# Optimization experiments

Measured on AMD Instinct MI355X. Metric: run time of the kernel, lower is better.

The kernel has to match this reference:

```python
import jax, jax.numpy as jnp
import numpy as np

SCOPE = 2
N = 20
D = 64
CAP = 32
IN_CH = 64
OUT_CH = 64
FIN_CH = 64
WIDTH = 2 * SCOPE + 1


def setup_inputs() -> dict:
    key = jax.random.key(0)
    ks = jax.random.split(key, 7)
    dm = 3 * CAP + D  # memory feature dim: 3 relpos blocks + spatial embedding

    def w(k, fan_in, shape):
        return jax.random.normal(k, shape, jnp.float32) / np.sqrt(fan_in)

    return dict(
        spatial_embeddings=jax.random.normal(ks[0], (N, N, N, D), jnp.float32),
        relpos_w=jax.random.normal(ks[1], (WIDTH, CAP), jnp.float32) / np.sqrt(WIDTH * CAP),
        Wq=w(ks[2], D, (D, IN_CH)), bq=jnp.zeros((IN_CH,), jnp.float32),
        Wk=w(ks[3], dm, (dm, IN_CH)), bk=jnp.zeros((IN_CH,), jnp.float32),
        Wv=w(ks[4], dm, (dm, OUT_CH)), bv=jnp.zeros((OUT_CH,), jnp.float32),
        Wo=w(ks[5], OUT_CH, (OUT_CH, FIN_CH)), bo=jnp.zeros((FIN_CH,), jnp.float32),
    )


def reference(spatial_embeddings, relpos_w, Wq, bq, Wk, bk, Wv, bv, Wo, bo):
    n = spatial_embeddings.shape[0]
    w = WIDTH
    m = n + 2 * SCOPE  # padded grid size
    cap = relpos_w.shape[-1]

    # within_edges=False: zero-pad all three spatial axes by SCOPE
    se = jnp.pad(spatial_embeddings, ((SCOPE, SCOPE),) * 3 + ((0, 0),))
    central = SCOPE + jnp.arange(n)               # padded centre indices [n]
    off = jnp.arange(-SCOPE, SCOPE + 1)           # [w]
    idx = central[:, None] + off[None, :]         # [n, w] padded neighbour indices

    # relative-position cube: relpos_cube[x,y,z] = concat(r[x], r[y], r[z])
    r0 = jnp.broadcast_to(relpos_w[:, None, None, :], (w, w, w, cap))
    r1 = jnp.broadcast_to(relpos_w[None, :, None, :], (w, w, w, cap))
    r2 = jnp.broadcast_to(relpos_w[None, None, :, :], (w, w, w, cap))
    relpos_flat = jnp.concatenate([r0, r1, r2], axis=-1).reshape(w * w * w, 3 * cap)

    # neighbour gather replicating jnp.meshgrid(...)'s default 'xy' indexing:
    # cube[b, a, c] = se[ni[a], nj[b], nk[c]]
    ii = idx[:, None, None, None, :, None]        # (qi, a)
    jj = idx[None, :, None, :, None, None]        # (qj, b)
    kk = idx[None, None, :, None, None, :]        # (qk, c)
    nb = se[ii, jj, kk]                           # [n,n,n,w,w,w,D]
    nb = nb.reshape(n, n, n, w * w * w, -1)       # [n,n,n,w^3,D]

    # keys/values over memory = concat(relpos, neighbours); split the weight
    Wk_rel, Wk_nb = Wk[:3 * cap], Wk[3 * cap:]
    Wv_rel, Wv_nb = Wv[:3 * cap], Wv[3 * cap:]
    k_rel = relpos_flat @ Wk_rel + bk             # [w^3, IN_CH] (query-independent)
    v_rel = relpos_flat @ Wv_rel + bv             # [w^3, OUT_CH]
    keys = k_rel + jnp.einsum('xyzpd,dc->xyzpc', nb, Wk_nb)
    values = v_rel + jnp.einsum('xyzpd,dc->xyzpc', nb, Wv_nb)

    # centre embedding at padded index `central` == original unpadded embedding
    q = spatial_embeddings @ Wq + bq              # [n,n,n,IN_CH]
    logits = jnp.einsum('xyzc,xyzpc->xyzp', q, keys)

    # edge mask, built in (a,b,c) cube order (faithful to original's flatten order)
    valid = ((idx > SCOPE) & (idx < m - SCOPE)).astype(logits.dtype)  # [n, w]
    mask = (valid[:, None, None, :, None, None]
            * valid[None, :, None, None, :, None]
            * valid[None, None, :, None, None, :]).reshape(n, n, n, w * w * w)
    logits = logits - (1.0 - mask) * 1e9

    scores = jax.nn.softmax(logits, axis=-1)
    reweighted = jnp.einsum('xyzp,xyzpc->xyzc', scores, values)
    return reweighted @ Wo + bo                   # [n,n,n,FIN_CH]
```

## Files before the change

### kernel.cpp

```cpp
#include <hip/hip_runtime.h>

#define NN 20
#define NP 125
#define NV (NN*NN*NN)

__global__ __launch_bounds__(64) void prep(
        const float* __restrict__ rpw,
        const float* __restrict__ Wk, const float* __restrict__ bk,
        const float* __restrict__ Wv, const float* __restrict__ bv,
        const float* __restrict__ Wo,
        float* __restrict__ k_rel, float* __restrict__ vrelW,
        float* __restrict__ Wvo) {
    const int c = threadIdx.x;
    if (blockIdx.x < NP) {
        const int p = blockIdx.x;
        const int d3 = p / 25, d4 = (p / 5) % 5, d5 = p % 5;
        __shared__ float vtmp[64];
        float ak = bk[c], av = bv[c];
#pragma unroll
        for (int t = 0; t < 96; ++t) {
            const int blk = t >> 5, off = t & 31;
            const int row = (blk == 0) ? d3 : (blk == 1) ? d4 : d5;
            const float r = rpw[row * 32 + off];
            ak = fmaf(r, Wk[t * 64 + c], ak);
            av = fmaf(r, Wv[t * 64 + c], av);
        }
        k_rel[p * 64 + c] = ak;
        vtmp[c] = av;
        __syncthreads();
        float o = 0.f;
#pragma unroll 8
        for (int e = 0; e < 64; ++e)
            o = fmaf(vtmp[e], Wo[e * 64 + c], o);
        vrelW[p * 64 + c] = o;
    } else {
        const int d = blockIdx.x - NP;
        float acc = 0.f;
#pragma unroll 8
        for (int e = 0; e < 64; ++e)
            acc = fmaf(Wv[(96 + d) * 64 + e], Wo[e * 64 + c], acc);
        Wvo[d * 64 + c] = acc;
    }
}

__global__ __launch_bounds__(256) void qkv2(
        const float* __restrict__ SE,
        const float* __restrict__ Wq, const float* __restrict__ bq,
        const float* __restrict__ Wk, const float* __restrict__ Wvo,
        float* __restrict__ Q, float* __restrict__ Km, float* __restrict__ VW) {
    __shared__ float se_s[32][65];
    const int t = threadIdx.x;
    const int vbase = blockIdx.x * 32;
    {
        const float4* __restrict__ src = (const float4*)(SE + vbase * 64);
        const float4 a = src[t];
        const float4 b = src[t + 256];
        const int r0 = t >> 4,        c0 = (t & 15) * 4;
        const int r1 = (t + 256) >> 4;
        se_s[r0][c0 + 0] = a.x; se_s[r0][c0 + 1] = a.y;
        se_s[r0][c0 + 2] = a.z; se_s[r0][c0 + 3] = a.w;
        se_s[r1][c0 + 0] = b.x; se_s[r1][c0 + 1] = b.y;
        se_s[r1][c0 + 2] = b.z; se_s[r1][c0 + 3] = b.w;
    }
    __syncthreads();
    const int lane = t & 63, w = t >> 6;
    float aq[8], ak[8], av[8];
#pragma unroll
    for (int j = 0; j < 8; ++j) { aq[j] = bq[lane]; ak[j] = 0.f; av[j] = 0.f; }
#pragma unroll 8
    for (int d = 0; d < 64; ++d) {
        const float wq = Wq[d * 64 + lane];
        const float wk = Wk[(96 + d) * 64 + lane];
        const float wv = Wvo[d * 64 + lane];
#pragma unroll
        for (int j = 0; j < 8; ++j) {
            const float s = se_s[w * 8 + j][d];
            aq[j] = fmaf(s, wq, aq[j]);
            ak[j] = fmaf(s, wk, ak[j]);
            av[j] = fmaf(s, wv, av[j]);
        }
    }
#pragma unroll
    for (int j = 0; j < 8; ++j) {
        const int v = vbase + w * 8 + j;
        Q[v * 64 + lane]  = aq[j];
        Km[v * 64 + lane] = ak[j];
        VW[v * 64 + lane] = av[j];
    }
}

__global__ __launch_bounds__(512, 4) void attn4(
        const float* __restrict__ Q, const float* __restrict__ Km,
        const float* __restrict__ VW,
        const float* __restrict__ k_rel, const float* __restrict__ vrelW,
        const float* __restrict__ bo,
        float* __restrict__ out) {
    __shared__ float u[216 * 65];
    __shared__ float sc_s[8][128];

    const int tid  = threadIdx.x;
    const int lane = tid & 63;
    const int w    = tid >> 6;

    const int chunk = blockIdx.x & 7;
    const int idx   = blockIdx.x >> 3;
    const int cx = chunk >> 2, cy = (chunk >> 1) & 1, cz = chunk & 1;
    const int TX = cx * 5 + idx / 25;
    const int TY = cy * 5 + (idx / 5) % 5;
    const int TZ = cz * 5 + idx % 5;

    const int wx = w >> 2, wy = (w >> 1) & 1, wz = w & 1;
    const int x = TX * 2 + wx, y = TY * 2 + wy, z = TZ * 2 + wz;
    const int v = (x * NN + y) * NN + z;

    for (int i = tid; i < 216 * 16; i += 512) {
        const int row = i >> 4, ch = i & 15;
        const int ux = row / 36, uy = (row / 6) % 6, uz = row % 6;
        const int gX = TX * 2 - 2 + ux;
        const int gY = TY * 2 - 2 + uy;
        const int gZ = TZ * 2 - 2 + uz;
        float4 val = make_float4(0.f, 0.f, 0.f, 0.f);
        if ((unsigned)gX <= 19u && (unsigned)gY <= 19u && (unsigned)gZ <= 19u)
            val = ((const float4*)Km)[((gX * NN + gY) * NN + gZ) * 16 + ch];
        const int b = row * 65 + ch * 4;
        u[b] = val.x; u[b + 1] = val.y; u[b + 2] = val.z; u[b + 3] = val.w;
    }

    const float q = Q[v * 64 + lane];
    const int p0 = lane;
    const int p1 = lane + 64;
    const int p1c = (p1 < NP) ? p1 : (NP - 1);

    int e3 = p0 / 25, e4 = (p0 / 5) % 5, e5 = p0 % 5;
    const int row0 = 36 * (wx + e4) + 6 * (wy + e3) + (wz + e5);
    const bool mv0 = ((unsigned)(x + e3 - 3) <= 18u) &&
                     ((unsigned)(y + e4 - 3) <= 18u) &&
                     ((unsigned)(z + e5 - 3) <= 18u);
    e3 = p1c / 25; e4 = (p1c / 5) % 5; e5 = p1c % 5;
    const int row1 = 36 * (wx + e4) + 6 * (wy + e3) + (wz + e5);
    const bool mv1 = (p1 < NP) &&
                     ((unsigned)(x + e3 - 3) <= 18u) &&
                     ((unsigned)(y + e4 - 3) <= 18u) &&
                     ((unsigned)(z + e5 - 3) <= 18u);

    const float4* __restrict__ kr0 = (const float4*)(k_rel + p0 * 64);
    const float4* __restrict__ kr1 = (const float4*)(k_rel + p1c * 64);

    __syncthreads();

    float a0 = 0.f, a1 = 0.f;
#pragma unroll
    for (int i = 0; i < 16; ++i) {
        const float qa = __shfl(q, 4 * i + 0);
        const float qb = __shfl(q, 4 * i + 1);
        const float qc = __shfl(q, 4 * i + 2);
        const float qd = __shfl(q, 4 * i + 3);
        const float4 r0 = kr0[i], r1 = kr1[i];
        const int b0 = row0 * 65 + 4 * i;
        const int b1 = row1 * 65 + 4 * i;
        a0 = fmaf(u[b0] + r0.x, qa, a0);
        a0 = fmaf(u[b0 + 1] + r0.y, qb, a0);
        a0 = fmaf(u[b0 + 2] + r0.z, qc, a0);
        a0 = fmaf(u[b0 + 3] + r0.w, qd, a0);
        a1 = fmaf(u[b1] + r1.x, qa, a1);
        a1 = fmaf(u[b1 + 1] + r1.y, qb, a1);
        a1 = fmaf(u[b1 + 2] + r1.z, qc, a1);
        a1 = fmaf(u[b1 + 3] + r1.w, qd, a1);
    }
    const float l0 = mv0 ? a0 : -1e9f;
    const float l1 = mv1 ? a1 : -1e9f;

    float m = fmaxf(l0, l1);
#pragma unroll
    for (int d = 1; d < 64; d <<= 1) m = fmaxf(m, __shfl_xor(m, d));
    const float e0 = __expf(l0 - m);
    const float e1 = __expf(l1 - m);
    float ssum = e0 + e1;
#pragma unroll
    for (int d = 1; d < 64; d <<= 1) ssum += __shfl_xor(ssum, d);
    const float inv = 1.f / ssum;
    sc_s[w][p0] = e0 * inv;
    sc_s[w][p1] = e1 * inv;
    __syncthreads();

    for (int i = tid; i < 216 * 16; i += 512) {
        const int row = i >> 4, ch = i & 15;
        const int ux = row / 36, uy = (row / 6) % 6, uz = row % 6;
        const int gX = TX * 2 - 2 + ux;
        const int gY = TY * 2 - 2 + uy;
        const int gZ = TZ * 2 - 2 + uz;
        float4 val = make_float4(0.f, 0.f, 0.f, 0.f);
        if ((unsigned)gX <= 19u && (unsigned)gY <= 19u && (unsigned)gZ <= 19u)
            val = ((const float4*)VW)[((gX * NN + gY) * NN + gZ) * 16 + ch];
        const int b = row * 65 + ch * 4;
        u[b] = val.x; u[b + 1] = val.y; u[b + 2] = val.z; u[b + 3] = val.w;
    }
    __syncthreads();

    float A0 = 0.f, A1 = 0.f, A2 = 0.f, A3 = 0.f, A4 = 0.f;
    const float* __restrict__ vr = vrelW + lane;
#pragma unroll 5
    for (int g = 0; g < 25; ++g) {
        const int ge3 = g / 5, ge4 = g % 5;
        const int rb = 36 * (wx + ge4) + 6 * (wy + ge3) + wz;
        const int pb = g * 5;
        A0 = fmaf(sc_s[w][pb + 0], u[(rb + 0) * 65 + lane] + vr[(pb + 0) * 64], A0);
        A1 = fmaf(sc_s[w][pb + 1], u[(rb + 1) * 65 + lane] + vr[(pb + 1) * 64], A1);
        A2 = fmaf(sc_s[w][pb + 2], u[(rb + 2) * 65 + lane] + vr[(pb + 2) * 64], A2);
        A3 = fmaf(sc_s[w][pb + 3], u[(rb + 3) * 65 + lane] + vr[(pb + 3) * 64], A3);
        A4 = fmaf(sc_s[w][pb + 4], u[(rb + 4) * 65 + lane] + vr[(pb + 4) * 64], A4);
    }
    const float rw = ((A0 + A1) + (A2 + A3)) + A4;
    out[v * 64 + lane] = rw + bo[lane];
}

extern "C" void kernel_launch(void* const* d_in, const int* in_sizes, int n_in,
                              void* d_out, int out_size, void* d_ws, size_t ws_size,
                              hipStream_t stream) {
    const float* SE  = (const float*)d_in[0];
    const float* rpw = (const float*)d_in[1];
    const float* Wq  = (const float*)d_in[2];
    const float* bq  = (const float*)d_in[3];
    const float* Wk  = (const float*)d_in[4];
    const float* bk  = (const float*)d_in[5];
    const float* Wv  = (const float*)d_in[6];
    const float* bv  = (const float*)d_in[7];
    const float* Wo  = (const float*)d_in[8];
    const float* bo  = (const float*)d_in[9];
    float* out = (float*)d_out;

    float* ws    = (float*)d_ws;
    float* Q     = ws;
    float* Km    = ws + 512000;
    float* VW    = ws + 1024000;
    float* k_rel = ws + 1536000;
    float* vrelW = ws + 1544000;
    float* Wvo   = ws + 1552000;

    prep<<<NP + 64, 64, 0, stream>>>(rpw, Wk, bk, Wv, bv, Wo, k_rel, vrelW, Wvo);
    qkv2<<<NV / 32, 256, 0, stream>>>(SE, Wq, bq, Wk, Wvo, Q, Km, VW);
    attn4<<<1000, 512, 0, stream>>>(Q, Km, VW, k_rel, vrelW, bo, out);
}
```

Baseline: 134.9 us.

## Merge prep and projection kernels; read neighbour values directly from global memory

The separate prep and qkv kernels become one launch. Each projection block recomputes the Wv·Wo product into shared memory, while the extra blocks compute k_rel and vrelW four positions per block. In the attention kernel, the shared-memory staging of the 216-row VW halo is dropped and each lane loads its neighbour values straight from global memory with bounds predicates. This removes a launch and a barrier plus the staging loop. In exchange, every block redundantly recomputes Wvo, and the value gather now relies on global/L2 traffic instead of shared memory.

```diff
diff --git a/kernel.cpp b/kernel.cpp
--- a/kernel.cpp
+++ b/kernel.cpp
@@ -4,92 +4,93 @@
 #define NP 125
 #define NV (NN*NN*NN)
 
-__global__ __launch_bounds__(64) void prep(
-        const float* __restrict__ rpw,
+__global__ __launch_bounds__(256) void pre(
+        const float* __restrict__ SE, const float* __restrict__ rpw,
+        const float* __restrict__ Wq, const float* __restrict__ bq,
         const float* __restrict__ Wk, const float* __restrict__ bk,
         const float* __restrict__ Wv, const float* __restrict__ bv,
         const float* __restrict__ Wo,
-        float* __restrict__ k_rel, float* __restrict__ vrelW,
-        float* __restrict__ Wvo) {
-    const int c = threadIdx.x;
-    if (blockIdx.x < NP) {
-        const int p = blockIdx.x;
-        const int d3 = p / 25, d4 = (p / 5) % 5, d5 = p % 5;
-        __shared__ float vtmp[64];
-        float ak = bk[c], av = bv[c];
-#pragma unroll
-        for (int t = 0; t < 96; ++t) {
-            const int blk = t >> 5, off = t & 31;
+        float* __restrict__ Q, float* __restrict__ Km, float* __restrict__ VW,
+        float* __restrict__ k_rel, float* __restrict__ vrelW) {
+    const int t = threadIdx.x;
+    const int lane = t & 63, w = t >> 6;
+
+    if (blockIdx.x < 500) {
+        __shared__ float se_s[16][65];
+        __shared__ float wvo_s[64 * 65];
+        const int vbase = blockIdx.x * 16;
+        {
+            const float4 a = ((const float4*)(SE + vbase * 64))[t];
+            const int r0 = t >> 4, c0 = (t & 15) * 4;
+            se_s[r0][c0 + 0] = a.x; se_s[r0][c0 + 1] = a.y;
+            se_s[r0][c0 + 2] = a.z; se_s[r0][c0 + 3] = a.w;
+        }
+        float acc[16];
+#pragma unroll
+        for (int k = 0; k < 16; ++k) acc[k] = 0.f;
+#pragma unroll 4
+        for (int e = 0; e < 64; ++e) {
+            const float wo = Wo[e * 64 + lane];
+#pragma unroll
+            for (int k = 0; k < 16; ++k)
+                acc[k] = fmaf(Wv[(96 + w * 16 + k) * 64 + e], wo, acc[k]);
+        }
+#pragma unroll
+        for (int k = 0; k < 16; ++k)
+            wvo_s[(w * 16 + k) * 65 + lane] = acc[k];
+        __syncthreads();
+
+        float aq[4], ak[4], av[4];
+#pragma unroll
+        for (int j = 0; j < 4; ++j) { aq[j] = bq[lane]; ak[j] = 0.f; av[j] = 0.f; }
+#pragma unroll 8
+        for (int d = 0; d < 64; ++d) {
+            const float wq = Wq[d * 64 + lane];
+            const float wk = Wk[(96 + d) * 64 + lane];
+            const float wv = wvo_s[d * 65 + lane];
+#pragma unroll
+            for (int j = 0; j < 4; ++j) {
+                const float s = se_s[w * 4 + j][d];
+                aq[j] = fmaf(s, wq, aq[j]);
+                ak[j] = fmaf(s, wk, ak[j]);
+                av[j] = fmaf(s, wv, av[j]);
+            }
+        }
+#pragma unroll
+        for (int j = 0; j < 4; ++j) {
+            const int v = vbase + w * 4 + j;
+            Q[v * 64 + lane]  = aq[j];
+            Km[v * 64 + lane] = ak[j];
+            VW[v * 64 + lane] = av[j];
+        }
+    } else {
+        __shared__ float vt[4][65];
+        const int p = (blockIdx.x - 500) * 4 + w;
+        const int pc = (p < NP) ? p : (NP - 1);
+        const int d3 = pc / 25, d4 = (pc / 5) % 5, d5 = pc % 5;
+        float ak = bk[lane], av = bv[lane];
+#pragma unroll
+        for (int tt = 0; tt < 96; ++tt) {
+            const int blk = tt >> 5, off = tt & 31;
             const int row = (blk == 0) ? d3 : (blk == 1) ? d4 : d5;
             const float r = rpw[row * 32 + off];
-            ak = fmaf(r, Wk[t * 64 + c], ak);
-            av = fmaf(r, Wv[t * 64 + c], av);
-        }
-        k_rel[p * 64 + c] = ak;
-        vtmp[c] = av;
+            ak = fmaf(r, Wk[tt * 64 + lane], ak);
+            av = fmaf(r, Wv[tt * 64 + lane], av);
+        }
+        vt[w][lane] = av;
         __syncthreads();
         float o = 0.f;
-#pragma unroll 8
+#pragma unroll 4
         for (int e = 0; e < 64; ++e)
-            o = fmaf(vtmp[e], Wo[e * 64 + c], o);
-        vrelW[p * 64 + c] = o;
-    } else {
-        const int d = blockIdx.x - NP;
-        float acc = 0.f;
-#pragma unroll 8
-        for (int e = 0; e < 64; ++e)
-            acc = fmaf(Wv[(96 + d) * 64 + e], Wo[e * 64 + c], acc);
-        Wvo[d * 64 + c] = acc;
+            o = fmaf(vt[w][e], Wo[e * 64 + lane], o);
+        if (p < NP) {
+            k_rel[p * 64 + lane] = ak;
+            vrelW[p * 64 + lane] = o;
+        }
     }
 }
 
-__global__ __launch_bounds__(256) void qkv2(
-        const float* __restrict__ SE,
-        const float* __restrict__ Wq, const float* __restrict__ bq,
-        const float* __restrict__ Wk, const float* __restrict__ Wvo,
-        float* __restrict__ Q, float* __restrict__ Km, float* __restrict__ VW) {
-    __shared__ float se_s[32][65];
-    const int t = threadIdx.x;
-    const int vbase = blockIdx.x * 32;
-    {
-        const float4* __restrict__ src = (const float4*)(SE + vbase * 64);
-        const float4 a = src[t];
-        const float4 b = src[t + 256];
-        const int r0 = t >> 4,        c0 = (t & 15) * 4;
-        const int r1 = (t + 256) >> 4;
-        se_s[r0][c0 + 0] = a.x; se_s[r0][c0 + 1] = a.y;
-        se_s[r0][c0 + 2] = a.z; se_s[r0][c0 + 3] = a.w;
-        se_s[r1][c0 + 0] = b.x; se_s[r1][c0 + 1] = b.y;
-        se_s[r1][c0 + 2] = b.z; se_s[r1][c0 + 3] = b.w;
-    }
-    __syncthreads();
-    const int lane = t & 63, w = t >> 6;
-    float aq[8], ak[8], av[8];
-#pragma unroll
-    for (int j = 0; j < 8; ++j) { aq[j] = bq[lane]; ak[j] = 0.f; av[j] = 0.f; }
-#pragma unroll 8
-    for (int d = 0; d < 64; ++d) {
-        const float wq = Wq[d * 64 + lane];
-        const float wk = Wk[(96 + d) * 64 + lane];
-        const float wv = Wvo[d * 64 + lane];
-#pragma unroll
-        for (int j = 0; j < 8; ++j) {
-            const float s = se_s[w * 8 + j][d];
-            aq[j] = fmaf(s, wq, aq[j]);
-            ak[j] = fmaf(s, wk, ak[j]);
-            av[j] = fmaf(s, wv, av[j]);
-        }
-    }
-#pragma unroll
-    for (int j = 0; j < 8; ++j) {
-        const int v = vbase + w * 8 + j;
-        Q[v * 64 + lane]  = aq[j];
-        Km[v * 64 + lane] = ak[j];
-        VW[v * 64 + lane] = av[j];
-    }
-}
-
-__global__ __launch_bounds__(512, 4) void attn4(
+__global__ __launch_bounds__(512, 4) void attn5(
         const float* __restrict__ Q, const float* __restrict__ Km,
         const float* __restrict__ VW,
         const float* __restrict__ k_rel, const float* __restrict__ vrelW,
@@ -183,32 +184,42 @@
     sc_s[w][p1] = e1 * inv;
     __syncthreads();
 
-    for (int i = tid; i < 216 * 16; i += 512) {
-        const int row = i >> 4, ch = i & 15;
-        const int ux = row / 36, uy = (row / 6) % 6, uz = row % 6;
-        const int gX = TX * 2 - 2 + ux;
-        const int gY = TY * 2 - 2 + uy;
-        const int gZ = TZ * 2 - 2 + uz;
-        float4 val = make_float4(0.f, 0.f, 0.f, 0.f);
-        if ((unsigned)gX <= 19u && (unsigned)gY <= 19u && (unsigned)gZ <= 19u)
-            val = ((const float4*)VW)[((gX * NN + gY) * NN + gZ) * 16 + ch];
-        const int b = row * 65 + ch * 4;
-        u[b] = val.x; u[b + 1] = val.y; u[b + 2] = val.z; u[b + 3] = val.w;
-    }
-    __syncthreads();
-
+    bool xin[5], yin[5], zin[5];
+#pragma unroll
+    for (int o = 0; o < 5; ++o) {
+        xin[o] = ((unsigned)(x + o - 2) <= 19u);
+        yin[o] = ((unsigned)(y + o - 2) <= 19u);
+        zin[o] = ((unsigned)(z + o - 2) <= 19u);
+    }
     float A0 = 0.f, A1 = 0.f, A2 = 0.f, A3 = 0.f, A4 = 0.f;
     const float* __restrict__ vr = vrelW + lane;
+    const float* __restrict__ vwl = VW + lane;
 #pragma unroll 5
     for (int g = 0; g < 25; ++g) {
         const int ge3 = g / 5, ge4 = g % 5;
-        const int rb = 36 * (wx + ge4) + 6 * (wy + ge3) + wz;
+        const int nbb = v + (ge4 - 2) * 400 + (ge3 - 2) * 20 - 2;
+        const bool xy = xin[ge4] && yin[ge3];
         const int pb = g * 5;
-        A0 = fmaf(sc_s[w][pb + 0], u[(rb + 0) * 65 + lane] + vr[(pb + 0) * 64], A0);
-        A1 = fmaf(sc_s[w][pb + 1], u[(rb + 1) * 65 + lane] + vr[(pb + 1) * 64], A1);
-        A2 = fmaf(sc_s[w][pb + 2], u[(rb + 2) * 65 + lane] + vr[(pb + 2) * 64], A2);
-        A3 = fmaf(sc_s[w][pb + 3], u[(rb + 3) * 65 + lane] + vr[(pb + 3) * 64], A3);
-        A4 = fmaf(sc_s[w][pb + 4], u[(rb + 4) * 65 + lane] + vr[(pb + 4) * 64], A4);
+        {
+            const float vm = (xy && zin[0]) ? vwl[(nbb + 0) * 64] : 0.f;
+            A0 = fmaf(sc_s[w][pb + 0], vr[(pb + 0) * 64] + vm, A0);
+        }
+        {
+            const float vm = (xy && zin[1]) ? vwl[(nbb + 1) * 64] : 0.f;
+            A1 = fmaf(sc_s[w][pb + 1], vr[(pb + 1) * 64] + vm, A1);
+        }
+        {
+            const float vm = (xy && zin[2]) ? vwl[(nbb + 2) * 64] : 0.f;
+            A2 = fmaf(sc_s[w][pb + 2], vr[(pb + 2) * 64] + vm, A2);
+        }
+        {
+            const float vm = (xy && zin[3]) ? vwl[(nbb + 3) * 64] : 0.f;
+            A3 = fmaf(sc_s[w][pb + 3], vr[(pb + 3) * 64] + vm, A3);
+        }
+        {
+            const float vm = (xy && zin[4]) ? vwl[(nbb + 4) * 64] : 0.f;
+            A4 = fmaf(sc_s[w][pb + 4], vr[(pb + 4) * 64] + vm, A4);
+        }
     }
     const float rw = ((A0 + A1) + (A2 + A3)) + A4;
     out[v * 64 + lane] = rw + bo[lane];
@@ -235,9 +246,8 @@
     float* VW    = ws + 1024000;
     float* k_rel = ws + 1536000;
     float* vrelW = ws + 1544000;
-    float* Wvo   = ws + 1552000;
-
-    prep<<<NP + 64, 64, 0, stream>>>(rpw, Wk, bk, Wv, bv, Wo, k_rel, vrelW, Wvo);
-    qkv2<<<NV / 32, 256, 0, stream>>>(SE, Wq, bq, Wk, Wvo, Q, Km, VW);
-    attn4<<<1000, 512, 0, stream>>>(Q, Km, VW, k_rel, vrelW, bo, out);
+
+    pre<<<532, 256, 0, stream>>>(SE, rpw, Wq, bq, Wk, bk, Wv, bv, Wo,
+                                 Q, Km, VW, k_rel, vrelW);
+    attn5<<<1000, 512, 0, stream>>>(Q, Km, VW, k_rel, vrelW, bo, out);
 }
```

Measured after the change: 151.8 us. +12.5%, slower.

## Split each voxel's 125 neighbours across two wavefronts with 1024-thread blocks

Applied to the files above, without the earlier changes.

The attention kernel now uses 1024 threads per block, so two wavefronts share each voxel. Each wavefront computes 64 of the 125 neighbour logits, and the softmax max and sum are combined across the pair through shared memory. The weighted value sum is split the same way, with the two halves added through shared memory before the store. This doubles thread-level parallelism and shortens each wave's serial work, at the cost of extra barriers, half-idle lanes in the second wave (61 of 64 used), and higher register pressure under launch_bounds(1024,2).

```diff
diff --git a/kernel.cpp b/kernel.cpp
--- a/kernel.cpp
+++ b/kernel.cpp
@@ -89,18 +89,21 @@
     }
 }
 
-__global__ __launch_bounds__(512, 4) void attn4(
+__global__ __launch_bounds__(1024, 2) void attn6(
         const float* __restrict__ Q, const float* __restrict__ Km,
         const float* __restrict__ VW,
         const float* __restrict__ k_rel, const float* __restrict__ vrelW,
         const float* __restrict__ bo,
         float* __restrict__ out) {
     __shared__ float u[216 * 65];
-    __shared__ float sc_s[8][128];
+    __shared__ float mred[16], sred[16];
+    __shared__ float prw[8][64];
 
     const int tid  = threadIdx.x;
     const int lane = tid & 63;
     const int w    = tid >> 6;
+    const int vox  = w & 7;
+    const int hi   = w >> 3;
 
     const int chunk = blockIdx.x & 7;
     const int idx   = blockIdx.x >> 3;
@@ -109,11 +112,11 @@
     const int TY = cy * 5 + (idx / 5) % 5;
     const int TZ = cz * 5 + idx % 5;
 
-    const int wx = w >> 2, wy = (w >> 1) & 1, wz = w & 1;
+    const int wx = vox >> 2, wy = (vox >> 1) & 1, wz = vox & 1;
     const int x = TX * 2 + wx, y = TY * 2 + wy, z = TZ * 2 + wz;
     const int v = (x * NN + y) * NN + z;
 
-    for (int i = tid; i < 216 * 16; i += 512) {
+    for (int i = tid; i < 216 * 16; i += 1024) {
         const int row = i >> 4, ch = i & 15;
         const int ux = row / 36, uy = (row / 6) % 6, uz = row % 6;
         const int gX = TX * 2 - 2 + ux;
@@ -127,63 +130,42 @@
     }
 
     const float q = Q[v * 64 + lane];
-    const int p0 = lane;
-    const int p1 = lane + 64;
-    const int p1c = (p1 < NP) ? p1 : (NP - 1);
-
-    int e3 = p0 / 25, e4 = (p0 / 5) % 5, e5 = p0 % 5;
-    const int row0 = 36 * (wx + e4) + 6 * (wy + e3) + (wz + e5);
-    const bool mv0 = ((unsigned)(x + e3 - 3) <= 18u) &&
-                     ((unsigned)(y + e4 - 3) <= 18u) &&
-                     ((unsigned)(z + e5 - 3) <= 18u);
-    e3 = p1c / 25; e4 = (p1c / 5) % 5; e5 = p1c % 5;
-    const int row1 = 36 * (wx + e4) + 6 * (wy + e3) + (wz + e5);
-    const bool mv1 = (p1 < NP) &&
-                     ((unsigned)(x + e3 - 3) <= 18u) &&
-                     ((unsigned)(y + e4 - 3) <= 18u) &&
-                     ((unsigned)(z + e5 - 3) <= 18u);
-
-    const float4* __restrict__ kr0 = (const float4*)(k_rel + p0 * 64);
-    const float4* __restrict__ kr1 = (const float4*)(k_rel + p1c * 64);
-
-    __syncthreads();
-
-    float a0 = 0.f, a1 = 0.f;
+
+    const int p  = lane + hi * 64;
+    const int pc = (p < NP) ? p : (NP - 1);
+    const int e3 = pc / 25, e4 = (pc / 5) % 5, e5 = pc % 5;
+    const int rowp = 36 * (wx + e4) + 6 * (wy + e3) + (wz + e5);
+    const bool mv = (p < NP) &&
+                    ((unsigned)(x + e3 - 3) <= 18u) &&
+                    ((unsigned)(y + e4 - 3) <= 18u) &&
+                    ((unsigned)(z + e5 - 3) <= 18u);
+    const float4* __restrict__ kr = (const float4*)(k_rel + pc * 64);
+
+    __syncthreads();
+
+    float a = 0.f;
 #pragma unroll
     for (int i = 0; i < 16; ++i) {
         const float qa = __shfl(q, 4 * i + 0);
         const float qb = __shfl(q, 4 * i + 1);
         const float qc = __shfl(q, 4 * i + 2);
         const float qd = __shfl(q, 4 * i + 3);
-        const float4 r0 = kr0[i], r1 = kr1[i];
-        const int b0 = row0 * 65 + 4 * i;
-        const int b1 = row1 * 65 + 4 * i;
-        a0 = fmaf(u[b0] + r0.x, qa, a0);
-        a0 = fmaf(u[b0 + 1] + r0.y, qb, a0);
-        a0 = fmaf(u[b0 + 2] + r0.z, qc, a0);
-        a0 = fmaf(u[b0 + 3] + r0.w, qd, a0);
-        a1 = fmaf(u[b1] + r1.x, qa, a1);
-        a1 = fmaf(u[b1 + 1] + r1.y, qb, a1);
-        a1 = fmaf(u[b1 + 2] + r1.z, qc, a1);
-        a1 = fmaf(u[b1 + 3] + r1.w, qd, a1);
-    }
-    const float l0 = mv0 ? a0 : -1e9f;
-    const float l1 = mv1 ? a1 : -1e9f;
-
-    float m = fmaxf(l0, l1);
+        const float4 r = kr[i];
+        const int b = rowp * 65 + 4 * i;
+        a = fmaf(u[b]     + r.x, qa, a);
+        a = fmaf(u[b + 1] + r.y, qb, a);
+        a = fmaf(u[b + 2] + r.z, qc, a);
+        a = fmaf(u[b + 3] + r.w, qd, a);
+    }
+    const float l = mv ? a : -1e9f;
+
+    float m = l;
 #pragma unroll
     for (int d = 1; d < 64; d <<= 1) m = fmaxf(m, __shfl_xor(m, d));
-    const float e0 = __expf(l0 - m);
-    const float e1 = __expf(l1 - m);
-    float ssum = e0 + e1;
-#pragma unroll
-    for (int d = 1; d < 64; d <<= 1) ssum += __shfl_xor(ssum, d);
-    const float inv = 1.f / ssum;
-    sc_s[w][p0] = e0 * inv;
-    sc_s[w][p1] = e1 * inv;
-    __syncthreads();
-
-    for (int i = tid; i < 216 * 16; i += 512) {
+    if (lane == 0) mred[w] = m;
+    __syncthreads();
+
+    for (int i = tid; i < 216 * 16; i += 1024) {
         const int row = i >> 4, ch = i & 15;
         const int ux = row / 36, uy = (row / 6) % 6, uz = row % 6;
         const int gX = TX * 2 - 2 + ux;
@@ -195,23 +177,46 @@
         const int b = row * 65 + ch * 4;
         u[b] = val.x; u[b + 1] = val.y; u[b + 2] = val.z; u[b + 3] = val.w;
     }
-    __syncthreads();
+
+    const float mm = fmaxf(mred[vox], mred[vox + 8]);
+    const float e  = __expf(l - mm);
+    float s = e;
+#pragma unroll
+    for (int d = 1; d < 64; d <<= 1) s += __shfl_xor(s, d);
+    if (lane == 0) sred[w] = s;
+    __syncthreads();
+
+    const float inv = 1.f / (sred[vox] + sred[vox + 8]);
+    const float sc_mine = e * inv;
 
     float A0 = 0.f, A1 = 0.f, A2 = 0.f, A3 = 0.f, A4 = 0.f;
     const float* __restrict__ vr = vrelW + lane;
-#pragma unroll 5
-    for (int g = 0; g < 25; ++g) {
-        const int ge3 = g / 5, ge4 = g % 5;
-        const int rb = 36 * (wx + ge4) + 6 * (wy + ge3) + wz;
-        const int pb = g * 5;
-        A0 = fmaf(sc_s[w][pb + 0], u[(rb + 0) * 65 + lane] + vr[(pb + 0) * 64], A0);
-        A1 = fmaf(sc_s[w][pb + 1], u[(rb + 1) * 65 + lane] + vr[(pb + 1) * 64], A1);
-        A2 = fmaf(sc_s[w][pb + 2], u[(rb + 2) * 65 + lane] + vr[(pb + 2) * 64], A2);
-        A3 = fmaf(sc_s[w][pb + 3], u[(rb + 3) * 65 + lane] + vr[(pb + 3) * 64], A3);
-        A4 = fmaf(sc_s[w][pb + 4], u[(rb + 4) * 65 + lane] + vr[(pb + 4) * 64], A4);
-    }
-    const float rw = ((A0 + A1) + (A2 + A3)) + A4;
-    out[v * 64 + lane] = rw + bo[lane];
+    if (hi == 0) {
+#pragma unroll
+        for (int pp = 0; pp < 64; ++pp) {
+            const int f3 = pp / 25, f4 = (pp / 5) % 5, f5 = pp % 5;
+            const int row = 36 * (wx + f4) + 6 * (wy + f3) + (wz + f5);
+            const float sc = __shfl(sc_mine, pp);
+            float& A = (pp % 5 == 0) ? A0 : (pp % 5 == 1) ? A1 :
+                       (pp % 5 == 2) ? A2 : (pp % 5 == 3) ? A3 : A4;
+            A = fmaf(sc, u[row * 65 + lane] + vr[pp * 64], A);
+        }
+    } else {
+#pragma unroll
+        for (int pp = 64; pp < NP; ++pp) {
+            const int f3 = pp / 25, f4 = (pp / 5) % 5, f5 = pp % 5;
+            const int row = 36 * (wx + f4) + 6 * (wy + f3) + (wz + f5);
+            const float sc = __shfl(sc_mine, pp - 64);
+            float& A = (pp % 5 == 0) ? A0 : (pp % 5 == 1) ? A1 :
+                       (pp % 5 == 2) ? A2 : (pp % 5 == 3) ? A3 : A4;
+            A = fmaf(sc, u[row * 65 + lane] + vr[pp * 64], A);
+        }
+    }
+    const float part = ((A0 + A1) + (A2 + A3)) + A4;
+    if (hi == 1) prw[vox][lane] = part;
+    __syncthreads();
+    if (hi == 0)
+        out[v * 64 + lane] = part + prw[vox][lane] + bo[lane];
 }
 
 extern "C" void kernel_launch(void* const* d_in, const int* in_sizes, int n_in,
@@ -239,5 +244,5 @@
 
     prep<<<NP + 64, 64, 0, stream>>>(rpw, Wk, bk, Wv, bv, Wo, k_rel, vrelW, Wvo);
     qkv2<<<NV / 32, 256, 0, stream>>>(SE, Wq, bq, Wk, Wvo, Q, Km, VW);
-    attn4<<<1000, 512, 0, stream>>>(Q, Km, VW, k_rel, vrelW, bo, out);
-}
+    attn6<<<1000, 1024, 0, stream>>>(Q, Km, VW, k_rel, vrelW, bo, out);
+}
```

Result: slower. 148.7 us (+10.3%).

## Precompute q·k_rel in projection kernel and score over 216 shared neighbour rows

Applied to the files above, without the earlier changes.

The q·k_rel term is now computed once per voxel in the projection kernel and written to a workspace buffer, so the attention kernel no longer adds relpos keys per element. Each wave computes dot products over all 216 rows of the shared key tile with float4 LDS reads (stride 68), and then maps them back to the 125 window positions through shuffles. Softmax scores stay in registers and are broadcast with readlane instead of passing through shared memory. In exchange, the projection kernel does extra work and more global writes (qkr is 128 floats per voxel), and the attention kernel does about 1.7x more dot-product FLOPs on out-of-window rows. Occupancy drops from launch bound 4 to 2.

```diff
diff --git a/kernel.cpp b/kernel.cpp
--- a/kernel.cpp
+++ b/kernel.cpp
@@ -3,6 +3,10 @@
 #define NN 20
 #define NP 125
 #define NV (NN*NN*NN)
+
+__device__ __forceinline__ float rlf(float v, int l) {
+    return __uint_as_float(__builtin_amdgcn_readlane(__float_as_uint(v), l));
+}
 
 __global__ __launch_bounds__(64) void prep(
         const float* __restrict__ rpw,
@@ -43,12 +47,15 @@
     }
 }
 
-__global__ __launch_bounds__(256) void qkv2(
+__global__ __launch_bounds__(256) void qkv3(
         const float* __restrict__ SE,
         const float* __restrict__ Wq, const float* __restrict__ bq,
         const float* __restrict__ Wk, const float* __restrict__ Wvo,
-        float* __restrict__ Q, float* __restrict__ Km, float* __restrict__ VW) {
+        const float* __restrict__ k_rel,
+        float* __restrict__ Q, float* __restrict__ Km, float* __restrict__ VW,
+        float* __restrict__ qkr) {
     __shared__ float se_s[32][65];
+    __shared__ float krs[125 * 65];
     const int t = threadIdx.x;
     const int vbase = blockIdx.x * 32;
     {
@@ -62,6 +69,12 @@
         se_s[r1][c0 + 0] = b.x; se_s[r1][c0 + 1] = b.y;
         se_s[r1][c0 + 2] = b.z; se_s[r1][c0 + 3] = b.w;
     }
+    for (int i = t; i < 125 * 16; i += 256) {
+        const int row = i >> 4, ch = i & 15;
+        const float4 val = ((const float4*)k_rel)[row * 16 + ch];
+        const int b = row * 65 + ch * 4;
+        krs[b] = val.x; krs[b + 1] = val.y; krs[b + 2] = val.z; krs[b + 3] = val.w;
+    }
     __syncthreads();
     const int lane = t & 63, w = t >> 6;
     float aq[8], ak[8], av[8];
@@ -87,16 +100,35 @@
         Km[v * 64 + lane] = ak[j];
         VW[v * 64 + lane] = av[j];
     }
-}
-
-__global__ __launch_bounds__(512, 4) void attn4(
+    const int p1c = (lane + 64 < NP) ? (lane + 64) : (NP - 1);
+#pragma unroll
+    for (int j = 0; j < 8; ++j) {
+        float d0 = 0.f, d1 = 0.f;
+#pragma unroll
+        for (int i = 0; i < 16; ++i) {
+            const float qa = rlf(aq[j], 4 * i + 0);
+            const float qb = rlf(aq[j], 4 * i + 1);
+            const float qc = rlf(aq[j], 4 * i + 2);
+            const float qd = rlf(aq[j], 4 * i + 3);
+            const int b0 = lane * 65 + 4 * i;
+            const int b1 = p1c * 65 + 4 * i;
+            d0 = fmaf(krs[b0], qa, d0); d0 = fmaf(krs[b0 + 1], qb, d0);
+            d0 = fmaf(krs[b0 + 2], qc, d0); d0 = fmaf(krs[b0 + 3], qd, d0);
+            d1 = fmaf(krs[b1], qa, d1); d1 = fmaf(krs[b1 + 1], qb, d1);
+            d1 = fmaf(krs[b1 + 2], qc, d1); d1 = fmaf(krs[b1 + 3], qd, d1);
+        }
+        const int v = vbase + w * 8 + j;
+        qkr[v * 128 + lane] = d0;
+        qkr[v * 128 + 64 + lane] = d1;
+    }
+}
+
+__global__ __launch_bounds__(512, 2) void attn7(
         const float* __restrict__ Q, const float* __restrict__ Km,
-        const float* __restrict__ VW,
-        const float* __restrict__ k_rel, const float* __restrict__ vrelW,
-        const float* __restrict__ bo,
+        const float* __restrict__ VW, const float* __restrict__ qkr,
+        const float* __restrict__ vrelW, const float* __restrict__ bo,
         float* __restrict__ out) {
-    __shared__ float u[216 * 65];
-    __shared__ float sc_s[8][128];
+    __shared__ __align__(16) float u[216 * 68];
 
     const int tid  = threadIdx.x;
     const int lane = tid & 63;
@@ -122,65 +154,90 @@
         float4 val = make_float4(0.f, 0.f, 0.f, 0.f);
         if ((unsigned)gX <= 19u && (unsigned)gY <= 19u && (unsigned)gZ <= 19u)
             val = ((const float4*)Km)[((gX * NN + gY) * NN + gZ) * 16 + ch];
-        const int b = row * 65 + ch * 4;
-        u[b] = val.x; u[b + 1] = val.y; u[b + 2] = val.z; u[b + 3] = val.w;
+        *(float4*)&u[row * 68 + ch * 4] = val;
     }
 
     const float q = Q[v * 64 + lane];
-    const int p0 = lane;
-    const int p1 = lane + 64;
-    const int p1c = (p1 < NP) ? p1 : (NP - 1);
-
-    int e3 = p0 / 25, e4 = (p0 / 5) % 5, e5 = p0 % 5;
-    const int row0 = 36 * (wx + e4) + 6 * (wy + e3) + (wz + e5);
-    const bool mv0 = ((unsigned)(x + e3 - 3) <= 18u) &&
-                     ((unsigned)(y + e4 - 3) <= 18u) &&
-                     ((unsigned)(z + e5 - 3) <= 18u);
-    e3 = p1c / 25; e4 = (p1c / 5) % 5; e5 = p1c % 5;
-    const int row1 = 36 * (wx + e4) + 6 * (wy + e3) + (wz + e5);
-    const bool mv1 = (p1 < NP) &&
-                     ((unsigned)(x + e3 - 3) <= 18u) &&
-                     ((unsigned)(y + e4 - 3) <= 18u) &&
-                     ((unsigned)(z + e5 - 3) <= 18u);
-
-    const float4* __restrict__ kr0 = (const float4*)(k_rel + p0 * 64);
-    const float4* __restrict__ kr1 = (const float4*)(k_rel + p1c * 64);
+
+    int   rr0, rr1, rr2, rr3;
+    float qk0, qk1, qk2, qk3;
+    bool  vd0, vd1, vd2, vd3;
+#define GEO(M, RR, QK, VD)                                                     \
+    {                                                                          \
+        const int r = lane + 64 * (M);                                         \
+        const bool okr = (r < 216);                                            \
+        const int rc = okr ? r : 0;                                            \
+        const int ux = rc / 36, uy = (rc / 6) % 6, uz = rc % 6;                \
+        const int E4 = ux - wx, E3 = uy - wy, E5 = uz - wz;                    \
+        const bool win = okr && (unsigned)E3 <= 4u && (unsigned)E4 <= 4u &&    \
+                         (unsigned)E5 <= 4u;                                   \
+        const bool mv = win && (unsigned)(x + E3 - 3) <= 18u &&                \
+                        (unsigned)(y + E4 - 3) <= 18u &&                       \
+                        (unsigned)(z + E5 - 3) <= 18u;                         \
+        const int p = 25 * E3 + 5 * E4 + E5;                                   \
+        RR = rc; VD = mv;                                                      \
+        QK = qkr[v * 128 + (mv ? p : 0)];                                      \
+    }
+    GEO(0, rr0, qk0, vd0)
+    GEO(1, rr1, qk1, vd1)
+    GEO(2, rr2, qk2, vd2)
+    GEO(3, rr3, qk3, vd3)
+#undef GEO
 
     __syncthreads();
 
-    float a0 = 0.f, a1 = 0.f;
+    float a0 = 0.f, a1 = 0.f, a2 = 0.f, a3 = 0.f;
 #pragma unroll
     for (int i = 0; i < 16; ++i) {
-        const float qa = __shfl(q, 4 * i + 0);
-        const float qb = __shfl(q, 4 * i + 1);
-        const float qc = __shfl(q, 4 * i + 2);
-        const float qd = __shfl(q, 4 * i + 3);
-        const float4 r0 = kr0[i], r1 = kr1[i];
-        const int b0 = row0 * 65 + 4 * i;
-        const int b1 = row1 * 65 + 4 * i;
-        a0 = fmaf(u[b0] + r0.x, qa, a0);
-        a0 = fmaf(u[b0 + 1] + r0.y, qb, a0);
-        a0 = fmaf(u[b0 + 2] + r0.z, qc, a0);
-        a0 = fmaf(u[b0 + 3] + r0.w, qd, a0);
-        a1 = fmaf(u[b1] + r1.x, qa, a1);
-        a1 = fmaf(u[b1 + 1] + r1.y, qb, a1);
-        a1 = fmaf(u[b1 + 2] + r1.z, qc, a1);
-        a1 = fmaf(u[b1 + 3] + r1.w, qd, a1);
-    }
-    const float l0 = mv0 ? a0 : -1e9f;
-    const float l1 = mv1 ? a1 : -1e9f;
-
-    float m = fmaxf(l0, l1);
-#pragma unroll
-    for (int d = 1; d < 64; d <<= 1) m = fmaxf(m, __shfl_xor(m, d));
-    const float e0 = __expf(l0 - m);
-    const float e1 = __expf(l1 - m);
-    float ssum = e0 + e1;
-#pragma unroll
-    for (int d = 1; d < 64; d <<= 1) ssum += __shfl_xor(ssum, d);
-    const float inv = 1.f / ssum;
-    sc_s[w][p0] = e0 * inv;
-    sc_s[w][p1] = e1 * inv;
+        const float qa = rlf(q, 4 * i + 0);
+        const float qb = rlf(q, 4 * i + 1);
+        const float qc = rlf(q, 4 * i + 2);
+        const float qd = rlf(q, 4 * i + 3);
+        const float4 k0 = *(const float4*)&u[rr0 * 68 + 4 * i];
+        const float4 k1 = *(const float4*)&u[rr1 * 68 + 4 * i];
+        const float4 k2 = *(const float4*)&u[rr2 * 68 + 4 * i];
+        const float4 k3 = *(const float4*)&u[rr3 * 68 + 4 * i];
+        a0 = fmaf(k0.x, qa, a0); a0 = fmaf(k0.y, qb, a0);
+        a0 = fmaf(k0.z, qc, a0); a0 = fmaf(k0.w, qd, a0);
+        a1 = fmaf(k1.x, qa, a1); a1 = fmaf(k1.y, qb, a1);
+        a1 = fmaf(k1.z, qc, a1); a1 = fmaf(k1.w, qd, a1);
+        a2 = fmaf(k2.x, qa, a2); a2 = fmaf(k2.y, qb, a2);
+        a2 = fmaf(k2.z, qc, a2); a2 = fmaf(k2.w, qd, a2);
+        a3 = fmaf(k3.x, qa, a3); a3 = fmaf(k3.y, qb, a3);
+        a3 = fmaf(k3.z, qc, a3); a3 = fmaf(k3.w, qd, a3);
+    }
+    const float l0 = vd0 ? a0 + qk0 : -1e9f;
+    const float l1 = vd1 ? a1 + qk1 : -1e9f;
+    const float l2 = vd2 ? a2 + qk2 : -1e9f;
+    const float l3 = vd3 ? a3 + qk3 : -1e9f;
+
+    float mm = fmaxf(fmaxf(l0, l1), fmaxf(l2, l3));
+#pragma unroll
+    for (int d = 1; d < 64; d <<= 1) mm = fmaxf(mm, __shfl_xor(mm, d));
+    const float e0 = __expf(l0 - mm);
+    const float e1 = __expf(l1 - mm);
+    const float e2 = __expf(l2 - mm);
+    const float e3v = __expf(l3 - mm);
+    float ss = ((e0 + e1) + (e2 + e3v));
+#pragma unroll
+    for (int d = 1; d < 64; d <<= 1) ss += __shfl_xor(ss, d);
+    const float inv = 1.f / ss;
+    const float sA = e0 * inv, sB = e1 * inv, sC = e2 * inv, sD = e3v * inv;
+
+    int d3 = lane / 25, d4 = (lane / 5) % 5, d5 = lane % 5;
+    const int r0 = 36 * (wx + d4) + 6 * (wy + d3) + (wz + d5);
+    const int p1c = (lane + 64 < NP) ? (lane + 64) : (NP - 1);
+    d3 = p1c / 25; d4 = (p1c / 5) % 5; d5 = p1c % 5;
+    const int r1 = 36 * (wx + d4) + 6 * (wy + d3) + (wz + d5);
+    const float cA0 = __shfl(sA, r0 & 63), cB0 = __shfl(sB, r0 & 63);
+    const float cC0 = __shfl(sC, r0 & 63), cD0 = __shfl(sD, r0 & 63);
+    const int sl0 = r0 >> 6;
+    const float s0 = (sl0 == 0) ? cA0 : (sl0 == 1) ? cB0 : (sl0 == 2) ? cC0 : cD0;
+    const float cA1 = __shfl(sA, r1 & 63), cB1 = __shfl(sB, r1 & 63);
+    const float cC1 = __shfl(sC, r1 & 63), cD1 = __shfl(sD, r1 & 63);
+    const int sl1 = r1 >> 6;
+    const float s1 = (sl1 == 0) ? cA1 : (sl1 == 1) ? cB1 : (sl1 == 2) ? cC1 : cD1;
+
     __syncthreads();
 
     for (int i = tid; i < 216 * 16; i += 512) {
@@ -192,8 +249,7 @@
         float4 val = make_float4(0.f, 0.f, 0.f, 0.f);
         if ((unsigned)gX <= 19u && (unsigned)gY <= 19u && (unsigned)gZ <= 19u)
             val = ((const float4*)VW)[((gX * NN + gY) * NN + gZ) * 16 + ch];
-        const int b = row * 65 + ch * 4;
-        u[b] = val.x; u[b + 1] = val.y; u[b + 2] = val.z; u[b + 3] = val.w;
+        *(float4*)&u[row * 68 + ch * 4] = val;
     }
     __syncthreads();
 
@@ -204,11 +260,14 @@
         const int ge3 = g / 5, ge4 = g % 5;
         const int rb = 36 * (wx + ge4) + 6 * (wy + ge3) + wz;
         const int pb = g * 5;
-        A0 = fmaf(sc_s[w][pb + 0], u[(rb + 0) * 65 + lane] + vr[(pb + 0) * 64], A0);
-        A1 = fmaf(sc_s[w][pb + 1], u[(rb + 1) * 65 + lane] + vr[(pb + 1) * 64], A1);
-        A2 = fmaf(sc_s[w][pb + 2], u[(rb + 2) * 65 + lane] + vr[(pb + 2) * 64], A2);
-        A3 = fmaf(sc_s[w][pb + 3], u[(rb + 3) * 65 + lane] + vr[(pb + 3) * 64], A3);
-        A4 = fmaf(sc_s[w][pb + 4], u[(rb + 4) * 65 + lane] + vr[(pb + 4) * 64], A4);
+#define STEP(J, ACC)                                                           \
+        {                                                                      \
+            const int p = pb + (J);                                            \
+            const float sc = (p < 64) ? rlf(s0, p) : rlf(s1, p - 64);          \
+            ACC = fmaf(sc, u[(rb + (J)) * 68 + lane] + vr[p * 64], ACC);       \
+        }
+        STEP(0, A0) STEP(1, A1) STEP(2, A2) STEP(3, A3) STEP(4, A4)
+#undef STEP
     }
     const float rw = ((A0 + A1) + (A2 + A3)) + A4;
     out[v * 64 + lane] = rw + bo[lane];
@@ -236,8 +295,9 @@
     float* k_rel = ws + 1536000;
     float* vrelW = ws + 1544000;
     float* Wvo   = ws + 1552000;
+    float* qkr   = ws + 1556096;
 
     prep<<<NP + 64, 64, 0, stream>>>(rpw, Wk, bk, Wv, bv, Wo, k_rel, vrelW, Wvo);
-    qkv2<<<NV / 32, 256, 0, stream>>>(SE, Wq, bq, Wk, Wvo, Q, Km, VW);
-    attn4<<<1000, 512, 0, stream>>>(Q, Km, VW, k_rel, vrelW, bo, out);
-}
+    qkv3<<<NV / 32, 256, 0, stream>>>(SE, Wq, bq, Wk, Wvo, k_rel, Q, Km, VW, qkr);
+    attn7<<<1000, 512, 0, stream>>>(Q, Km, VW, qkr, vrelW, bo, out);
+}
```

New measurement: 137.6 us. No clear change (+2.0%).
